# Optimization experiments

Measured on AMD Instinct MI355X. Metric: run time of the kernel, lower is better.

Reference implementation:

```python
import jax, jax.numpy as jnp
import numpy as np
from jax import lax

KH, KW = 3, 3
CIN, F = 32, 32
WSIZE = KH * KW * CIN * F  # 9216


def setup_inputs() -> dict:
    key = jax.random.key(0)
    k1, k2 = jax.random.split(key)
    x = jax.random.normal(k1, (32, 128, 128, CIN), dtype=jnp.float32)
    # hypernetwork output: per-sample flattened kernel (+ bias)
    params = jax.random.normal(k2, (32, WSIZE + F), dtype=jnp.float32) * 0.05
    return {"x": x, "params": params}


def reference(x, params):
    B = x.shape[0]
    # kernel_shape = (kh, kw, input_dim, filters) per keras channels_last
    W = params[:, :WSIZE].reshape(B, KH, KW, CIN, F)  # [B, kh, kw, Cin, F]
    b = params[:, WSIZE:]                              # [B, F]

    def conv_one(xi, wi, bi):
        # xi: [H, W, Cin], wi: [kh, kw, Cin, F] (HWIO), bi: [F]
        out = lax.conv_general_dilated(
            xi[None], wi,
            window_strides=(1, 1), padding="SAME",
            dimension_numbers=("NHWC", "HWIO", "NHWC"),
        )
        return out[0] + bi  # broadcast bias over H, W

    # per-sample dynamic convolution, vectorized over batch
    return jax.vmap(conv_one)(x, W, b)  # activation=None -> linear
```

## Files before the change

kernel.cpp:

```cpp
#include <hip/hip_runtime.h>


typedef __attribute__((ext_vector_type(8))) short bf16x8;
typedef __attribute__((ext_vector_type(4))) float f32x4;

constexpr int HWD  = 128, CINC = 32, FC = 32;
constexpr int WSZ  = 9 * CINC * FC;
constexpr int PSTR = WSZ + FC;
constexpr int XS_BYTES = 4 * 4 * 130 * 16;
constexpr int WT_BYTES = 36 * 32 * 16;
constexpr int SMEM_BYTES = XS_BYTES + WT_BYTES;

__device__ __forceinline__ int xs_off(int cig, int r, int col) {
    return ((cig * 4 + r) * 130 + col) * 16;
}
__device__ __forceinline__ int wt_off(int kgrp, int f) {
    return XS_BYTES + (kgrp * 32 + f) * 16;
}

__device__ __forceinline__ unsigned short f2bf(float f) {
    unsigned u = __float_as_uint(f);
    return (unsigned short)((u + 0x7FFFu + ((u >> 16) & 1u)) >> 16);
}
__device__ __forceinline__ bf16x8 pack8(float4 a, float4 b) {
    bf16x8 r;
    r[0] = (short)f2bf(a.x); r[1] = (short)f2bf(a.y);
    r[2] = (short)f2bf(a.z); r[3] = (short)f2bf(a.w);
    r[4] = (short)f2bf(b.x); r[5] = (short)f2bf(b.y);
    r[6] = (short)f2bf(b.z); r[7] = (short)f2bf(b.w);
    return r;
}

__global__ __launch_bounds__(256) void conv3x3_mfma(
    const float* __restrict__ x, const float* __restrict__ params,
    float* __restrict__ out)
{
    __shared__ __align__(16) unsigned char smem[SMEM_BYTES];

    const int hw      = blockIdx.x;
    const int logical = (hw & 7) * 256 + (hw >> 3);
    const int b       = logical >> 6;
    const int rowpair = logical & 63;
    const int y0      = rowpair * 2;

    const int t = threadIdx.x;
    const float* __restrict__ xb = x + (size_t)b * (HWD * HWD * CINC);
    const float* __restrict__ pw = params + (size_t)b * PSTR;

    for (int i = t; i < 4 * 4 * 130; i += 256) {
        bf16x8 z = 0;
        *(bf16x8*)(smem + i * 16) = z;
    }
    __syncthreads();

    #pragma unroll
    for (int i = 0; i < 8; ++i) {
        const int c   = t + i * 256;
        const int r   = c >> 9;
        const int rem = c & 511;
        const int col = rem >> 2;
        const int cig = rem & 3;
        const int iy  = y0 - 1 + r;
        if (iy >= 0 && iy < HWD) {
            const float* p = xb + ((size_t)iy * HWD + col) * CINC + cig * 8;
            const float4 v0 = *(const float4*)(p);
            const float4 v1 = *(const float4*)(p + 4);
            *(bf16x8*)(smem + xs_off(cig, r, col + 1)) = pack8(v0, v1);
        }
    }

    #pragma unroll
    for (int j = 0; j < 5; ++j) {
        const int c    = t + j * 256;
        const int kgrp = c >> 5;
        const int f    = c & 31;
        if (kgrp < 36) {
            const float* p = pw + (size_t)(kgrp * 8) * FC + f;
            float4 a, bb;
            a.x  = p[0 * FC]; a.y  = p[1 * FC]; a.z  = p[2 * FC]; a.w  = p[3 * FC];
            bb.x = p[4 * FC]; bb.y = p[5 * FC]; bb.z = p[6 * FC]; bb.w = p[7 * FC];
            *(bf16x8*)(smem + wt_off(kgrp, f)) = pack8(a, bb);
        }
    }
    __syncthreads();

    const int wv   = t >> 6;
    const int ln   = t & 63;
    const int lg   = ln >> 4;
    const int li   = ln & 15;
    const int yloc = wv >> 1;
    const int xw   = (wv & 1) * 64;

    f32x4 acc[4][2];
    #pragma unroll
    for (int i = 0; i < 4; ++i) {
        acc[i][0] = (f32x4)0.0f;
        acc[i][1] = (f32x4)0.0f;
    }

    #pragma unroll
    for (int kh = 0; kh < 3; ++kh) {
        #pragma unroll
        for (int kw = 0; kw < 3; ++kw) {
            const int s = kh * 3 + kw;
            const bf16x8 b0 = *(const bf16x8*)(smem + wt_off(s * 4 + lg, li));
            const bf16x8 b1 = *(const bf16x8*)(smem + wt_off(s * 4 + lg, 16 + li));
            const int r = yloc + kh;
            const int colbase = xw + li + kw;
            #pragma unroll
            for (int tI = 0; tI < 4; ++tI) {
                const bf16x8 a = *(const bf16x8*)(smem + xs_off(lg, r, colbase + tI * 16));
                acc[tI][0] = __builtin_amdgcn_mfma_f32_16x16x32_bf16(a, b0, acc[tI][0], 0, 0, 0);
                acc[tI][1] = __builtin_amdgcn_mfma_f32_16x16x32_bf16(a, b1, acc[tI][1], 0, 0, 0);
            }
        }
    }

    const float bias0 = pw[WSZ + li];
    const float bias1 = pw[WSZ + 16 + li];
    const int yo = y0 + yloc;
    float* __restrict__ ob = out + ((size_t)(b * HWD + yo)) * (HWD * FC);

    #pragma unroll
    for (int tI = 0; tI < 4; ++tI) {
        #pragma unroll
        for (int reg = 0; reg < 4; ++reg) {
            const int px = xw + tI * 16 + lg * 4 + reg;
            float* q = ob + (size_t)px * FC;
            q[li]      = acc[tI][0][reg] + bias0;
            q[16 + li] = acc[tI][1][reg] + bias1;
        }
    }
}

extern "C" void kernel_launch(void* const* d_in, const int* in_sizes, int n_in,
                              void* d_out, int out_size, void* d_ws, size_t ws_size,
                              hipStream_t stream)
{
    const float* x      = (const float*)d_in[0];
    const float* params = (const float*)d_in[1];
    float*       out    = (float*)d_out;

    dim3 grid(2048);
    dim3 block(256);
    hipLaunchKernelGGL(conv3x3_mfma, grid, block, 0, stream, x, params, out);
}
```

Baseline: 126.0 us.

## Pre-pack per-sample weights to bf16 workspace and stream fragments from global

Adds a small prep kernel that converts each sample's weights into bf16 MFMA fragments in the workspace once. The conv kernel then reads those fragments from global memory with a one-step prefetch instead of staging them in LDS. This removes the 32x redundant per-block weight conversion and frees LDS for higher occupancy. It also folds the zero-fill into the input load pass, dropping one barrier, and pads each channel-group plane in LDS to avoid bank conflicts. The cost is an extra kernel launch, and the weight reads now go through global memory and cache instead of LDS.

```diff
diff --git a/kernel.cpp b/kernel.cpp
--- a/kernel.cpp
+++ b/kernel.cpp
@@ -7,12 +7,16 @@
 constexpr int HWD  = 128, CINC = 32, FC = 32;
 constexpr int WSZ  = 9 * CINC * FC;
 constexpr int PSTR = WSZ + FC;
-constexpr int XS_BYTES = 4 * 4 * 130 * 16;
-constexpr int WT_BYTES = 36 * 32 * 16;
-constexpr int SMEM_BYTES = XS_BYTES + WT_BYTES;
+
+constexpr int XS_PLANE  = 4 * 130 * 16;
+constexpr int XS_BYTES  = 4 * (XS_PLANE + 32);
+constexpr int WT_BYTES  = 36 * 32 * 16;
+
+constexpr size_t WS_FRAGS = 32ull * 36 * 32;
+constexpr size_t WS_NEED  = WS_FRAGS * 16;
 
 __device__ __forceinline__ int xs_off(int cig, int r, int col) {
-    return ((cig * 4 + r) * 130 + col) * 16;
+    return ((cig * 4 + r) * 130 + col) * 16 + cig * 32;
 }
 __device__ __forceinline__ int wt_off(int kgrp, int f) {
     return XS_BYTES + (kgrp * 32 + f) * 16;
@@ -31,55 +35,76 @@
     return r;
 }
 
-__global__ __launch_bounds__(256) void conv3x3_mfma(
+__global__ __launch_bounds__(256) void wprep(
+    const float* __restrict__ params, bf16x8* __restrict__ ws)
+{
+    const int b   = blockIdx.y;
+    const int seg = blockIdx.x;
+    const float* __restrict__ pw = params + (size_t)b * PSTR;
+    #pragma unroll
+    for (int i = 0; i < 2; ++i) {
+        const int idx = threadIdx.x + i * 256;
+        if (idx < 288) {
+            const int c  = seg * 288 + idx;
+            const int sg = c >> 5;
+            const int f  = c & 31;
+            const float* p = pw + (size_t)(sg * 8) * FC + f;
+            float4 a, bb;
+            a.x  = p[0 * FC]; a.y  = p[1 * FC]; a.z  = p[2 * FC]; a.w  = p[3 * FC];
+            bb.x = p[4 * FC]; bb.y = p[5 * FC]; bb.z = p[6 * FC]; bb.w = p[7 * FC];
+            ws[(size_t)b * 1152 + c] = pack8(a, bb);
+        }
+    }
+}
+
+template<bool USE_WS>
+__global__ __launch_bounds__(256, USE_WS ? 4 : 3) void conv3x3_mfma(
     const float* __restrict__ x, const float* __restrict__ params,
-    float* __restrict__ out)
+    float* __restrict__ out, const bf16x8* __restrict__ ws)
 {
-    __shared__ __align__(16) unsigned char smem[SMEM_BYTES];
+    __shared__ __align__(16) unsigned char smem[XS_BYTES + (USE_WS ? 0 : WT_BYTES)];
 
     const int hw      = blockIdx.x;
     const int logical = (hw & 7) * 256 + (hw >> 3);
     const int b       = logical >> 6;
-    const int rowpair = logical & 63;
-    const int y0      = rowpair * 2;
+    const int y0      = (logical & 63) * 2;
 
     const int t = threadIdx.x;
     const float* __restrict__ xb = x + (size_t)b * (HWD * HWD * CINC);
     const float* __restrict__ pw = params + (size_t)b * PSTR;
 
-    for (int i = t; i < 4 * 4 * 130; i += 256) {
-        bf16x8 z = 0;
-        *(bf16x8*)(smem + i * 16) = z;
-    }
-    __syncthreads();
-
     #pragma unroll
-    for (int i = 0; i < 8; ++i) {
-        const int c   = t + i * 256;
-        const int r   = c >> 9;
-        const int rem = c & 511;
-        const int col = rem >> 2;
-        const int cig = rem & 3;
-        const int iy  = y0 - 1 + r;
-        if (iy >= 0 && iy < HWD) {
-            const float* p = xb + ((size_t)iy * HWD + col) * CINC + cig * 8;
-            const float4 v0 = *(const float4*)(p);
-            const float4 v1 = *(const float4*)(p + 4);
-            *(bf16x8*)(smem + xs_off(cig, r, col + 1)) = pack8(v0, v1);
+    for (int i = 0; i < 9; ++i) {
+        const int c = t + i * 256;
+        if (c < 2080) {
+            const int cig      = c & 3;
+            const unsigned q   = (unsigned)(c >> 2);
+            const unsigned r   = q / 130u;
+            const unsigned col = q - r * 130u;
+            const int iy   = y0 - 1 + (int)r;
+            const int icol = (int)col - 1;
+            bf16x8 v = 0;
+            if ((unsigned)iy < 128u && (unsigned)icol < 128u) {
+                const float* p = xb + ((size_t)iy * HWD + icol) * CINC + cig * 8;
+                v = pack8(*(const float4*)(p), *(const float4*)(p + 4));
+            }
+            *(bf16x8*)(smem + xs_off(cig, (int)r, (int)col)) = v;
         }
     }
 
-    #pragma unroll
-    for (int j = 0; j < 5; ++j) {
-        const int c    = t + j * 256;
-        const int kgrp = c >> 5;
-        const int f    = c & 31;
-        if (kgrp < 36) {
-            const float* p = pw + (size_t)(kgrp * 8) * FC + f;
-            float4 a, bb;
-            a.x  = p[0 * FC]; a.y  = p[1 * FC]; a.z  = p[2 * FC]; a.w  = p[3 * FC];
-            bb.x = p[4 * FC]; bb.y = p[5 * FC]; bb.z = p[6 * FC]; bb.w = p[7 * FC];
-            *(bf16x8*)(smem + wt_off(kgrp, f)) = pack8(a, bb);
+    if constexpr (!USE_WS) {
+        #pragma unroll
+        for (int j = 0; j < 5; ++j) {
+            const int c    = t + j * 256;
+            const int kgrp = c >> 5;
+            const int f    = c & 31;
+            if (kgrp < 36) {
+                const float* p = pw + (size_t)(kgrp * 8) * FC + f;
+                float4 a, bb;
+                a.x  = p[0 * FC]; a.y  = p[1 * FC]; a.z  = p[2 * FC]; a.w  = p[3 * FC];
+                bb.x = p[4 * FC]; bb.y = p[5 * FC]; bb.z = p[6 * FC]; bb.w = p[7 * FC];
+                *(bf16x8*)(smem + wt_off(kgrp, f)) = pack8(a, bb);
+            }
         }
     }
     __syncthreads();
@@ -93,27 +118,39 @@
 
     f32x4 acc[4][2];
     #pragma unroll
-    for (int i = 0; i < 4; ++i) {
-        acc[i][0] = (f32x4)0.0f;
-        acc[i][1] = (f32x4)0.0f;
+    for (int i = 0; i < 4; ++i) { acc[i][0] = (f32x4)0.0f; acc[i][1] = (f32x4)0.0f; }
+
+    const size_t wsb = (size_t)b * 1152 + lg * 32;
+
+    bf16x8 bc0, bc1;
+    if constexpr (USE_WS) {
+        bc0 = ws[wsb + li];
+        bc1 = ws[wsb + 16 + li];
     }
 
     #pragma unroll
-    for (int kh = 0; kh < 3; ++kh) {
+    for (int s = 0; s < 9; ++s) {
+        const int kh = s / 3, kw = s % 3;
+        bf16x8 b0, b1, bn0, bn1;
+        if constexpr (USE_WS) {
+            if (s < 8) {
+                bn0 = ws[wsb + (s + 1) * 128 + li];
+                bn1 = ws[wsb + (s + 1) * 128 + 16 + li];
+            }
+            b0 = bc0; b1 = bc1;
+        } else {
+            b0 = *(const bf16x8*)(smem + wt_off(s * 4 + lg, li));
+            b1 = *(const bf16x8*)(smem + wt_off(s * 4 + lg, 16 + li));
+        }
+        const int r = yloc + kh;
+        const int colbase = xw + li + kw;
         #pragma unroll
-        for (int kw = 0; kw < 3; ++kw) {
-            const int s = kh * 3 + kw;
-            const bf16x8 b0 = *(const bf16x8*)(smem + wt_off(s * 4 + lg, li));
-            const bf16x8 b1 = *(const bf16x8*)(smem + wt_off(s * 4 + lg, 16 + li));
-            const int r = yloc + kh;
-            const int colbase = xw + li + kw;
-            #pragma unroll
-            for (int tI = 0; tI < 4; ++tI) {
-                const bf16x8 a = *(const bf16x8*)(smem + xs_off(lg, r, colbase + tI * 16));
-                acc[tI][0] = __builtin_amdgcn_mfma_f32_16x16x32_bf16(a, b0, acc[tI][0], 0, 0, 0);
-                acc[tI][1] = __builtin_amdgcn_mfma_f32_16x16x32_bf16(a, b1, acc[tI][1], 0, 0, 0);
-            }
+        for (int tI = 0; tI < 4; ++tI) {
+            const bf16x8 a = *(const bf16x8*)(smem + xs_off(lg, r, colbase + tI * 16));
+            acc[tI][0] = __builtin_amdgcn_mfma_f32_16x16x32_bf16(a, b0, acc[tI][0], 0, 0, 0);
+            acc[tI][1] = __builtin_amdgcn_mfma_f32_16x16x32_bf16(a, b1, acc[tI][1], 0, 0, 0);
         }
+        if constexpr (USE_WS) { bc0 = bn0; bc1 = bn1; }
     }
 
     const float bias0 = pw[WSZ + li];
@@ -141,7 +178,13 @@
     const float* params = (const float*)d_in[1];
     float*       out    = (float*)d_out;
 
-    dim3 grid(2048);
-    dim3 block(256);
-    hipLaunchKernelGGL(conv3x3_mfma, grid, block, 0, stream, x, params, out);
+    if (ws_size >= WS_NEED && d_ws != nullptr) {
+        bf16x8* ws = (bf16x8*)d_ws;
+        hipLaunchKernelGGL(wprep, dim3(4, 32), dim3(256), 0, stream, params, ws);
+        hipLaunchKernelGGL((conv3x3_mfma<true>), dim3(2048), dim3(256), 0, stream,
+                           x, params, out, (const bf16x8*)ws);
+    } else {
+        hipLaunchKernelGGL((conv3x3_mfma<false>), dim3(2048), dim3(256), 0, stream,
+                           x, params, out, (const bf16x8*)nullptr);
+    }
 }
```

After: 127.1 us. Within noise of the previous version (+0.8%).
